# Performance work log

Hardware: AMD Instinct MI355X
Metric: run time of the kernel (lower is better)

## Reference

```python
import jax, jax.numpy as jnp
import numpy as np
import math

C = 512
D = C // 4  # 128
SCALE = math.sqrt(D)

def setup_inputs() -> dict:
    key = jax.random.key(0)
    k1, k2, k3, k4 = jax.random.split(key, 4)
    x = jax.random.normal(k1, (8, C, 2048), dtype=jnp.float32)
    # q_conv and k_conv share the same weight (tied in the torch module)
    wqk = jax.random.normal(k2, (D, C), dtype=jnp.float32) * (1.0 / math.sqrt(C))
    wv = jax.random.normal(k3, (D, C), dtype=jnp.float32) * (1.0 / math.sqrt(C))
    bv = jax.random.normal(k4, (D,), dtype=jnp.float32) * 0.01
    return {"x": x, "wqk": wqk, "wv": wv, "bv": bv}

def reference(x, wqk, wv, bv):
    # x: [B, C, N]; 1x1 conv == matmul over channel dim
    xq = jnp.einsum('dc,bcn->bnd', wqk, x)          # [B, N, D]
    xk = jnp.einsum('dc,bcn->bdn', wqk, x)          # [B, D, N]
    xv = jnp.einsum('dc,bcn->bdn', wv, x) + bv[None, :, None]  # [B, D, N]
    energy = jnp.einsum('bnd,bdm->bnm', xq, xk) / SCALE  # [B, N, N]
    attention = jax.nn.softmax(energy, axis=-1)
    x_r = jnp.einsum('bdn,bnm->bdm', xv, attention)  # [B, D, N]
    return x_r
```

## Files before the change

### kernel.cpp

```cpp
#include <hip/hip_runtime.h>

typedef short short4v __attribute__((ext_vector_type(4)));
typedef short short8 __attribute__((ext_vector_type(8)));
typedef float floatx4 __attribute__((ext_vector_type(4)));
typedef unsigned int uint;
typedef unsigned short ushort;

#define CH 512
#define NN 2048
#define DD 128
#define RSCALE 0.08838834764831845f

__device__ __forceinline__ float bf2f(ushort u) {
    union { uint i; float f; } v; v.i = ((uint)u) << 16; return v.f;
}
__device__ __forceinline__ ushort f2bf(float f) {
    union { float f; uint u; } v; v.f = f;
    uint u = v.u;
    return (ushort)((u + 0x7fffu + ((u >> 16) & 1u)) >> 16);
}

__global__ void k0_zero(float* __restrict__ lsum) {
    lsum[blockIdx.x * 256 + threadIdx.x] = 0.0f;
}

__global__ __launch_bounds__(256) void k0_wconv(
    const float* __restrict__ wqk, const float* __restrict__ wv,
    ushort* __restrict__ Wbf)
{
    int gid = blockIdx.x * 256 + threadIdx.x;
    int base = gid * 4;
    const float* src = (base < 65536) ? (wqk + base) : (wv + base - 65536);
    float4 v = *(const float4*)src;
    short4v o;
    o[0] = (short)f2bf(v.x); o[1] = (short)f2bf(v.y);
    o[2] = (short)f2bf(v.z); o[3] = (short)f2bf(v.w);
    *(short4v*)&Wbf[base] = o;
}

__global__ __launch_bounds__(256) void k1_proj(
    const float* __restrict__ x,
    const ushort* __restrict__ Wbf,
    const float* __restrict__ bv,
    ushort* __restrict__ Q,
    ushort* __restrict__ V)
{
    const int nt = blockIdx.x;
    const int b  = blockIdx.y;
    const int n0 = nt * 32;
    const int t = threadIdx.x;
    const int lane = t & 63, w = t >> 6, l15 = lane & 15, quad = lane >> 4;

    __shared__ __attribute__((aligned(16))) ushort As[32 * 40];
    __shared__ __attribute__((aligned(16))) ushort Bs[256 * 40];

    floatx4 acc[2][4];
#pragma unroll
    for (int i = 0; i < 2; i++)
#pragma unroll
        for (int j = 0; j < 4; j++) acc[i][j] = (floatx4)(0.0f);

    const float* xb = x + b * (CH * NN) + n0;

    for (int c0 = 0; c0 < CH; c0 += 32) {
        {
            int n = t & 31, g = t >> 5;
            short4v v;
#pragma unroll
            for (int i = 0; i < 4; i++)
                v[i] = (short)f2bf(xb[(c0 + g * 4 + i) * NN + n]);
            *(short4v*)&As[n * 40 + g * 4] = v;
        }
#pragma unroll
        for (int rep = 0; rep < 16; rep++) {
            int idx = rep * 256 + t;
            int row = idx >> 4, cp = idx & 15;
            *(uint*)&Bs[row * 40 + cp * 2] = *(const uint*)&Wbf[row * CH + c0 + cp * 2];
        }
        __syncthreads();
        short8 a0 = *(short8*)&As[(l15) * 40 + quad * 8];
        short8 a1 = *(short8*)&As[(16 + l15) * 40 + quad * 8];
#pragma unroll
        for (int dt2 = 0; dt2 < 4; dt2++) {
            short8 bf = *(short8*)&Bs[(w * 64 + dt2 * 16 + l15) * 40 + quad * 8];
            acc[0][dt2] = __builtin_amdgcn_mfma_f32_16x16x32_bf16(a0, bf, acc[0][dt2], 0, 0, 0);
            acc[1][dt2] = __builtin_amdgcn_mfma_f32_16x16x32_bf16(a1, bf, acc[1][dt2], 0, 0, 0);
        }
        __syncthreads();
    }
#pragma unroll
    for (int ns = 0; ns < 2; ns++)
#pragma unroll
        for (int dt2 = 0; dt2 < 4; dt2++) {
            int ds_ = w * 64 + dt2 * 16 + l15;
#pragma unroll
            for (int r = 0; r < 4; r++) {
                int n = n0 + ns * 16 + quad * 4 + r;
                float val = acc[ns][dt2][r];
                if (ds_ < 128) {
                    Q[b * (NN * DD) + n * DD + ds_] = f2bf(val);
                } else {
                    int dv = ds_ - 128;
                    V[b * (NN * DD) + n * DD + dv] = f2bf(val + bv[dv]);
                }
            }
        }
}

__global__ __launch_bounds__(256) void k2_qqt(
    const ushort* __restrict__ Q,
    ushort* __restrict__ Pg,
    float* __restrict__ lsum)
{
    const int it = blockIdx.x;
    const int jt = blockIdx.y;
    const int b  = blockIdx.z;
    const int i0 = it * 128, j0 = jt * 64;
    const int t = threadIdx.x;
    const int lane = t & 63, w = t >> 6, l15 = lane & 15, quad = lane >> 4;
    const int wi = (w >> 1) * 64, wj = (w & 1) * 32;

    __shared__ __attribute__((aligned(16))) ushort Qi[128 * 136];
    __shared__ __attribute__((aligned(16))) ushort Qj[64 * 136];

    const ushort* Qb = Q + b * (NN * DD);

#pragma unroll
    for (int rep = 0; rep < 8; rep++) {
        int idx = rep * 256 + t;
        int row = idx >> 4, g = idx & 15;
        *(short8*)&Qi[row * 136 + g * 8] = *(const short8*)&Qb[(i0 + row) * DD + g * 8];
    }
#pragma unroll
    for (int rep = 0; rep < 4; rep++) {
        int idx = rep * 256 + t;
        int row = idx >> 4, g = idx & 15;
        *(short8*)&Qj[row * 136 + g * 8] = *(const short8*)&Qb[(j0 + row) * DD + g * 8];
    }
    __syncthreads();

    floatx4 acc[4][2];
#pragma unroll
    for (int i = 0; i < 4; i++)
#pragma unroll
        for (int j = 0; j < 2; j++) acc[i][j] = (floatx4)(0.0f);

#pragma unroll
    for (int kd = 0; kd < 4; kd++) {
        short8 afr[4], bfr[2];
#pragma unroll
        for (int nt = 0; nt < 4; nt++)
            afr[nt] = *(short8*)&Qi[(wi + nt * 16 + l15) * 136 + kd * 32 + quad * 8];
#pragma unroll
        for (int mt = 0; mt < 2; mt++)
            bfr[mt] = *(short8*)&Qj[(wj + mt * 16 + l15) * 136 + kd * 32 + quad * 8];
#pragma unroll
        for (int nt = 0; nt < 4; nt++)
#pragma unroll
            for (int mt = 0; mt < 2; mt++)
                acc[nt][mt] = __builtin_amdgcn_mfma_f32_16x16x32_bf16(afr[nt], bfr[mt], acc[nt][mt], 0, 0, 0);
    }

    ushort* Pb = Pg + (size_t)b * NN * NN;
#pragma unroll
    for (int nt = 0; nt < 4; nt++) {
        float rs[4] = {0.f, 0.f, 0.f, 0.f};
#pragma unroll
        for (int mt = 0; mt < 2; mt++) {
#pragma unroll
            for (int r = 0; r < 4; r++) {
                float p = __expf(acc[nt][mt][r] * RSCALE);
                rs[r] += p;
                Pb[(size_t)(i0 + wi + nt * 16 + quad * 4 + r) * NN + (j0 + wj + mt * 16 + l15)] = f2bf(p);
            }
        }
#pragma unroll
        for (int r = 0; r < 4; r++) {
            float s = rs[r];
            s += __shfl_xor(s, 1);
            s += __shfl_xor(s, 2);
            s += __shfl_xor(s, 4);
            s += __shfl_xor(s, 8);
            if (l15 == 0)
                atomicAdd(&lsum[b * NN + i0 + wi + nt * 16 + quad * 4 + r], s);
        }
    }
}

__global__ __launch_bounds__(256) void k2_scale_t(
    const ushort* __restrict__ V,
    const float* __restrict__ lsum,
    ushort* __restrict__ VT)
{
    const int nt = blockIdx.x;
    const int b = blockIdx.y;
    const int n0 = nt * 64;
    const int t = threadIdx.x;

    __shared__ __attribute__((aligned(16))) ushort Vt[64 * 132];

    const ushort* Vb = V + b * (NN * DD);
#pragma unroll
    for (int rep = 0; rep < 16; rep++) {
        int idx = rep * 256 + t;
        int row = idx >> 6, dp = idx & 63;
        *(uint*)&Vt[row * 132 + dp * 2] = *(const uint*)&Vb[(n0 + row) * DD + dp * 2];
    }
    __syncthreads();
#pragma unroll
    for (int rep = 0; rep < 16; rep++) {
        int idx = rep * 256 + t;
        int d = idx >> 5, col2 = idx & 31;
        int n = n0 + col2 * 2;
        float l0 = 1.0f / lsum[b * NN + n], l1 = 1.0f / lsum[b * NN + n + 1];
        float v0 = bf2f(Vt[(col2 * 2) * 132 + d]) * l0;
        float v1 = bf2f(Vt[(col2 * 2 + 1) * 132 + d]) * l1;
        uint pack = (uint)f2bf(v0) | ((uint)f2bf(v1) << 16);
        *(uint*)&VT[(size_t)b * DD * NN + (size_t)d * NN + n] = pack;
    }
}

__global__ __launch_bounds__(256) void k3_gemm(
    const ushort* __restrict__ VT,
    const ushort* __restrict__ Pg,
    float* __restrict__ out)
{
    const int mt2 = blockIdx.x;
    const int b = blockIdx.y;
    const int m0 = mt2 * 32;
    const int t = threadIdx.x;
    const int lane = t & 63, w = t >> 6, l15 = lane & 15, quad = lane >> 4;

    __shared__ __attribute__((aligned(16))) ushort As2[128 * 72];
    __shared__ __attribute__((aligned(16))) ushort Ps2[32 * 72];

    const ushort* VTb = VT + (size_t)b * DD * NN;
    const ushort* Pb = Pg + (size_t)b * NN * NN;

    floatx4 acc[2][2];
#pragma unroll
    for (int i = 0; i < 2; i++)
#pragma unroll
        for (int j = 0; j < 2; j++) acc[i][j] = (floatx4)(0.0f);

    for (int n0c = 0; n0c < NN; n0c += 64) {
#pragma unroll
        for (int rep = 0; rep < 16; rep++) {
            int idx = rep * 256 + t;
            int row = idx >> 5, col2 = idx & 31;
            *(uint*)&As2[row * 72 + col2 * 2] = *(const uint*)&VTb[(size_t)row * NN + n0c + col2 * 2];
        }
#pragma unroll
        for (int rep = 0; rep < 4; rep++) {
            int idx = rep * 256 + t;
            int row = idx >> 5, col2 = idx & 31;
            *(uint*)&Ps2[row * 72 + col2 * 2] = *(const uint*)&Pb[(size_t)(m0 + row) * NN + n0c + col2 * 2];
        }
        __syncthreads();
#pragma unroll
        for (int kn = 0; kn < 2; kn++) {
            short8 pb0 = *(short8*)&Ps2[(l15) * 72 + kn * 32 + quad * 8];
            short8 pb1 = *(short8*)&Ps2[(16 + l15) * 72 + kn * 32 + quad * 8];
#pragma unroll
            for (int sub = 0; sub < 2; sub++) {
                short8 va = *(short8*)&As2[(w * 32 + sub * 16 + l15) * 72 + kn * 32 + quad * 8];
                acc[sub][0] = __builtin_amdgcn_mfma_f32_16x16x32_bf16(va, pb0, acc[sub][0], 0, 0, 0);
                acc[sub][1] = __builtin_amdgcn_mfma_f32_16x16x32_bf16(va, pb1, acc[sub][1], 0, 0, 0);
            }
        }
        __syncthreads();
    }

    float* ob = out + (size_t)b * DD * NN;
#pragma unroll
    for (int sub = 0; sub < 2; sub++)
#pragma unroll
        for (int mtk = 0; mtk < 2; mtk++)
#pragma unroll
            for (int r = 0; r < 4; r++) {
                int d = w * 32 + sub * 16 + quad * 4 + r;
                int m = m0 + mtk * 16 + l15;
                ob[(size_t)d * NN + m] = acc[sub][mtk][r];
            }
}

__global__ __launch_bounds__(256) void k1_fb(
    const float* __restrict__ x, const float* __restrict__ wqk,
    const float* __restrict__ wv, const float* __restrict__ bv,
    ushort* __restrict__ Q, ushort* __restrict__ V)
{
    const int nt = blockIdx.x;
    const int b  = blockIdx.y;
    const int n0 = nt * 32;
    const int t = threadIdx.x;
    const int lane = t & 63, w = t >> 6, l15 = lane & 15, quad = lane >> 4;

    __shared__ __attribute__((aligned(16))) ushort As[32 * 40];
    __shared__ __attribute__((aligned(16))) ushort Bs[256 * 40];

    floatx4 acc[2][4];
#pragma unroll
    for (int i = 0; i < 2; i++)
#pragma unroll
        for (int j = 0; j < 4; j++) acc[i][j] = (floatx4)(0.0f);

    const float* xb = x + b * (CH * NN) + n0;

    for (int c0 = 0; c0 < CH; c0 += 32) {
        {
            int n = t & 31, g = t >> 5;
            short4v v;
#pragma unroll
            for (int i = 0; i < 4; i++)
                v[i] = (short)f2bf(xb[(c0 + g * 4 + i) * NN + n]);
            *(short4v*)&As[n * 40 + g * 4] = v;
        }
#pragma unroll
        for (int rep = 0; rep < 16; rep++) {
            int idx = rep * 256 + t;
            int row = idx >> 4, cp = idx & 15;
            const float* wf = (row < 128) ? (wqk + row * CH) : (wv + (row - 128) * CH);
            uint pack = (uint)f2bf(wf[c0 + cp * 2]) | ((uint)f2bf(wf[c0 + cp * 2 + 1]) << 16);
            *(uint*)&Bs[row * 40 + cp * 2] = pack;
        }
        __syncthreads();
        short8 a0 = *(short8*)&As[(l15) * 40 + quad * 8];
        short8 a1 = *(short8*)&As[(16 + l15) * 40 + quad * 8];
#pragma unroll
        for (int dt2 = 0; dt2 < 4; dt2++) {
            short8 bf = *(short8*)&Bs[(w * 64 + dt2 * 16 + l15) * 40 + quad * 8];
            acc[0][dt2] = __builtin_amdgcn_mfma_f32_16x16x32_bf16(a0, bf, acc[0][dt2], 0, 0, 0);
            acc[1][dt2] = __builtin_amdgcn_mfma_f32_16x16x32_bf16(a1, bf, acc[1][dt2], 0, 0, 0);
        }
        __syncthreads();
    }
#pragma unroll
    for (int ns = 0; ns < 2; ns++)
#pragma unroll
        for (int dt2 = 0; dt2 < 4; dt2++) {
            int ds_ = w * 64 + dt2 * 16 + l15;
#pragma unroll
            for (int r = 0; r < 4; r++) {
                int n = n0 + ns * 16 + quad * 4 + r;
                float val = acc[ns][dt2][r];
                if (ds_ < 128) {
                    Q[b * (NN * DD) + n * DD + ds_] = f2bf(val);
                } else {
                    int dv = ds_ - 128;
                    V[b * (NN * DD) + n * DD + dv] = f2bf(val + bv[dv]);
                }
            }
        }
}

__global__ __launch_bounds__(256) void k2_norm(
    const ushort* __restrict__ Q, ushort* __restrict__ V)
{
    const int ntile = blockIdx.x;
    const int b = blockIdx.y;
    const int n0 = ntile * 64;
    const int t = threadIdx.x;
    const int lane = t & 63, w = t >> 6, l15 = lane & 15, quad = lane >> 4;

    __shared__ __attribute__((aligned(16))) ushort Qs[64 * 136];
    __shared__ __attribute__((aligned(16))) ushort Qm[64 * 136];

    const ushort* Qb = Q + b * (NN * DD);

#pragma unroll
    for (int rep = 0; rep < 16; rep++) {
        int idx = rep * 256 + t;
        int row = idx >> 6, dp = idx & 63;
        *(uint*)&Qs[row * 136 + dp * 2] = *(const uint*)&Qb[(n0 + row) * DD + dp * 2];
    }
    __syncthreads();

    short8 afr[4];
#pragma unroll
    for (int kd = 0; kd < 4; kd++)
        afr[kd] = *(short8*)&Qs[(w * 16 + l15) * 136 + kd * 32 + quad * 8];

    float sums[4] = {0.f, 0.f, 0.f, 0.f};

    for (int m0 = 0; m0 < NN; m0 += 64) {
#pragma unroll
        for (int rep = 0; rep < 16; rep++) {
            int idx = rep * 256 + t;
            int row = idx >> 6, dp = idx & 63;
            *(uint*)&Qm[row * 136 + dp * 2] = *(const uint*)&Qb[(m0 + row) * DD + dp * 2];
        }
        __syncthreads();
#pragma unroll
        for (int ct = 0; ct < 4; ct++) {
            floatx4 s = (floatx4)(0.0f);
#pragma unroll
            for (int kd = 0; kd < 4; kd++) {
                short8 bf = *(short8*)&Qm[(ct * 16 + l15) * 136 + kd * 32 + quad * 8];
                s = __builtin_amdgcn_mfma_f32_16x16x32_bf16(afr[kd], bf, s, 0, 0, 0);
            }
#pragma unroll
            for (int r = 0; r < 4; r++)
                sums[r] += __expf(s[r] * RSCALE);
        }
        __syncthreads();
    }

#pragma unroll
    for (int r = 0; r < 4; r++) {
        float s = sums[r];
        s += __shfl_xor(s, 1);
        s += __shfl_xor(s, 2);
        s += __shfl_xor(s, 4);
        s += __shfl_xor(s, 8);
        sums[r] = s;
    }

    ushort* Vb = V + b * (NN * DD);
#pragma unroll
    for (int r = 0; r < 4; r++) {
        int n = n0 + w * 16 + quad * 4 + r;
        float inv = 1.0f / sums[r];
        short8 vv = *(short8*)&Vb[n * DD + l15 * 8];
        short8 o;
#pragma unroll
        for (int i = 0; i < 8; i++)
            o[i] = (short)f2bf(bf2f((ushort)vv[i]) * inv);
        *(short8*)&Vb[n * DD + l15 * 8] = o;
    }
}

__global__ __launch_bounds__(256) void k3_attn(
    const ushort* __restrict__ Q, const ushort* __restrict__ Vp,
    float* __restrict__ out)
{
    const int mtile = blockIdx.x;
    const int b = blockIdx.y;
    const int m0 = mtile * 64;
    const int t = threadIdx.x;
    const int lane = t & 63, w = t >> 6, l15 = lane & 15, quad = lane >> 4;

    __shared__ __attribute__((aligned(16))) ushort Qs[64 * 136];
    __shared__ __attribute__((aligned(16))) ushort Qn[32 * 136];
    __shared__ __attribute__((aligned(16))) ushort Vs[128 * 40];
    __shared__ __attribute__((aligned(16))) ushort Ps[64 * 40];

    const ushort* Qb = Q + b * (NN * DD);
    const ushort* Vpb = Vp + b * (NN * DD);

#pragma unroll
    for (int rep = 0; rep < 16; rep++) {
        int idx = rep * 256 + t;
        int row = idx >> 6, dp = idx & 63;
        *(uint*)&Qs[row * 136 + dp * 2] = *(const uint*)&Qb[(m0 + row) * DD + dp * 2];
    }
    __syncthreads();

    short8 afr[4];
#pragma unroll
    for (int kd = 0; kd < 4; kd++)
        afr[kd] = *(short8*)&Qs[(w * 16 + l15) * 136 + kd * 32 + quad * 8];

    floatx4 acc[2][4];
#pragma unroll
    for (int s = 0; s < 2; s++)
#pragma unroll
        for (int mt = 0; mt < 4; mt++) acc[s][mt] = (floatx4)(0.0f);

    for (int n0c = 0; n0c < NN; n0c += 32) {
#pragma unroll
        for (int rep = 0; rep < 8; rep++) {
            int idx = rep * 256 + t;
            int row = idx >> 6, dp = idx & 63;
            *(uint*)&Qn[row * 136 + dp * 2] = *(const uint*)&Qb[(n0c + row) * DD + dp * 2];
        }
#pragma unroll
        for (int rep = 0; rep < 8; rep++) {
            int idx = rep * 256 + t;
            int np = idx >> 7, d = idx & 127;
            uint v0 = Vpb[(n0c + np * 2) * DD + d];
            uint v1 = Vpb[(n0c + np * 2 + 1) * DD + d];
            *(uint*)&Vs[d * 40 + np * 2] = v0 | (v1 << 16);
        }
        __syncthreads();

#pragma unroll
        for (int nt2 = 0; nt2 < 2; nt2++) {
            floatx4 s = (floatx4)(0.0f);
#pragma unroll
            for (int kd = 0; kd < 4; kd++) {
                short8 bf = *(short8*)&Qn[(nt2 * 16 + l15) * 136 + kd * 32 + quad * 8];
                s = __builtin_amdgcn_mfma_f32_16x16x32_bf16(afr[kd], bf, s, 0, 0, 0);
            }
#pragma unroll
            for (int r = 0; r < 4; r++) {
                float p = __expf(s[r] * RSCALE);
                Ps[(w * 16 + quad * 4 + r) * 40 + nt2 * 16 + l15] = f2bf(p);
            }
        }
        __syncthreads();

        short8 pb[4];
#pragma unroll
        for (int mt = 0; mt < 4; mt++)
            pb[mt] = *(short8*)&Ps[(mt * 16 + l15) * 40 + quad * 8];
#pragma unroll
        for (int sub = 0; sub < 2; sub++) {
            short8 va = *(short8*)&Vs[(w * 32 + sub * 16 + l15) * 40 + quad * 8];
#pragma unroll
            for (int mt = 0; mt < 4; mt++)
                acc[sub][mt] = __builtin_amdgcn_mfma_f32_16x16x32_bf16(va, pb[mt], acc[sub][mt], 0, 0, 0);
        }
        __syncthreads();
    }

    float* ob = out + (size_t)b * DD * NN;
#pragma unroll
    for (int sub = 0; sub < 2; sub++)
#pragma unroll
        for (int mt = 0; mt < 4; mt++)
#pragma unroll
            for (int r = 0; r < 4; r++) {
                int d = w * 32 + sub * 16 + quad * 4 + r;
                int m = m0 + mt * 16 + l15;
                ob[(size_t)d * NN + m] = acc[sub][mt][r];
            }
}

extern "C" void kernel_launch(void* const* d_in, const int* in_sizes, int n_in,
                              void* d_out, int out_size, void* d_ws, size_t ws_size,
                              hipStream_t stream) {
    const float* x   = (const float*)d_in[0];
    const float* wqk = (const float*)d_in[1];
    const float* wv  = (const float*)d_in[2];
    const float* bv  = (const float*)d_in[3];
    float* out = (float*)d_out;

    ushort* Q = (ushort*)d_ws;
    ushort* V = (ushort*)((char*)d_ws + (4u << 20));

    if (ws_size >= (size_t)80 * 1024 * 1024) {
        ushort* Wbf  = (ushort*)((char*)d_ws + (8u << 20));
        float*  lsum = (float*)((char*)d_ws + (8u << 20) + (256u << 10));
        ushort* VT   = (ushort*)((char*)d_ws + (12u << 20));
        ushort* Pg   = (ushort*)((char*)d_ws + (16u << 20));

        k0_zero<<<64, 256, 0, stream>>>(lsum);
        k0_wconv<<<128, 256, 0, stream>>>(wqk, wv, Wbf);
        k1_proj<<<dim3(64, 8), 256, 0, stream>>>(x, Wbf, bv, Q, V);
        k2_qqt<<<dim3(16, 32, 8), 256, 0, stream>>>(Q, Pg, lsum);
        k2_scale_t<<<dim3(32, 8), 256, 0, stream>>>(V, lsum, VT);
        k3_gemm<<<dim3(64, 8), 256, 0, stream>>>(VT, Pg, out);
    } else {
        k1_fb<<<dim3(64, 8), 256, 0, stream>>>(x, wqk, wv, bv, Q, V);
        k2_norm<<<dim3(32, 8), 256, 0, stream>>>(Q, V);
        k3_attn<<<dim3(32, 8), 256, 0, stream>>>(Q, V, out);
    }
}
```

Baseline: 182.0 us.

## Recompute exp(QQ^T) in fused PV kernel instead of materializing P

The row-sum kernel now only computes the softmax normalizers and no longer writes the full bf16 probability matrix (8x2048x2048) to global memory. The final GEMM kernel recomputes the Q·Q^T tile and its exponentials on the fly in shared memory and multiplies them by the pre-scaled V^T, which avoids the large write and read-back of P. The cost is computing the energy matmul and exp twice. The workspace threshold for the fast path drops because the P buffer is gone.

New measurement: 191.7 us. 5.3% more time.

```diff
diff --git a/kernel.cpp b/kernel.cpp
--- a/kernel.cpp
+++ b/kernel.cpp
@@ -107,9 +107,8 @@
         }
 }
 
-__global__ __launch_bounds__(256) void k2_qqt(
+__global__ __launch_bounds__(256) void kl_sum(
     const ushort* __restrict__ Q,
-    ushort* __restrict__ Pg,
     float* __restrict__ lsum)
 {
     const int it = blockIdx.x;
@@ -161,19 +160,14 @@
                 acc[nt][mt] = __builtin_amdgcn_mfma_f32_16x16x32_bf16(afr[nt], bfr[mt], acc[nt][mt], 0, 0, 0);
     }
 
-    ushort* Pb = Pg + (size_t)b * NN * NN;
 #pragma unroll
     for (int nt = 0; nt < 4; nt++) {
         float rs[4] = {0.f, 0.f, 0.f, 0.f};
 #pragma unroll
-        for (int mt = 0; mt < 2; mt++) {
-#pragma unroll
-            for (int r = 0; r < 4; r++) {
-                float p = __expf(acc[nt][mt][r] * RSCALE);
-                rs[r] += p;
-                Pb[(size_t)(i0 + wi + nt * 16 + quad * 4 + r) * NN + (j0 + wj + mt * 16 + l15)] = f2bf(p);
-            }
-        }
+        for (int mt = 0; mt < 2; mt++)
+#pragma unroll
+            for (int r = 0; r < 4; r++)
+                rs[r] += __expf(acc[nt][mt][r] * RSCALE);
 #pragma unroll
         for (int r = 0; r < 4; r++) {
             float s = rs[r];
@@ -220,22 +214,39 @@
     }
 }
 
-__global__ __launch_bounds__(256) void k3_gemm(
+__global__ __launch_bounds__(256) void k_fused(
+    const ushort* __restrict__ Q,
     const ushort* __restrict__ VT,
-    const ushort* __restrict__ Pg,
     float* __restrict__ out)
 {
-    const int mt2 = blockIdx.x;
+    const int mt = blockIdx.x;
     const int b = blockIdx.y;
-    const int m0 = mt2 * 32;
+    const int m0 = mt * 32;
     const int t = threadIdx.x;
     const int lane = t & 63, w = t >> 6, l15 = lane & 15, quad = lane >> 4;
 
-    __shared__ __attribute__((aligned(16))) ushort As2[128 * 72];
-    __shared__ __attribute__((aligned(16))) ushort Ps2[32 * 72];
-
+    __shared__ __attribute__((aligned(16))) ushort Qm[32 * 136];
+    __shared__ __attribute__((aligned(16))) ushort Qn[64 * 136];
+    __shared__ __attribute__((aligned(16))) ushort Vs[128 * 72];
+    __shared__ __attribute__((aligned(16))) ushort Ps[32 * 68];
+
+    const ushort* Qb = Q + b * (NN * DD);
     const ushort* VTb = VT + (size_t)b * DD * NN;
-    const ushort* Pb = Pg + (size_t)b * NN * NN;
+
+#pragma unroll
+    for (int rep = 0; rep < 2; rep++) {
+        int idx = rep * 256 + t;
+        int row = idx >> 4, g = idx & 15;
+        *(short8*)&Qm[row * 136 + g * 8] = *(const short8*)&Qb[(m0 + row) * DD + g * 8];
+    }
+    __syncthreads();
+
+    short8 qm[2][4];
+#pragma unroll
+    for (int ms = 0; ms < 2; ms++)
+#pragma unroll
+        for (int kd = 0; kd < 4; kd++)
+            qm[ms][kd] = *(short8*)&Qm[(ms * 16 + l15) * 136 + kd * 32 + quad * 8];
 
     floatx4 acc[2][2];
 #pragma unroll
@@ -244,44 +255,59 @@
         for (int j = 0; j < 2; j++) acc[i][j] = (floatx4)(0.0f);
 
     for (int n0c = 0; n0c < NN; n0c += 64) {
-#pragma unroll
-        for (int rep = 0; rep < 16; rep++) {
-            int idx = rep * 256 + t;
-            int row = idx >> 5, col2 = idx & 31;
-            *(uint*)&As2[row * 72 + col2 * 2] = *(const uint*)&VTb[(size_t)row * NN + n0c + col2 * 2];
-        }
+        __syncthreads();
 #pragma unroll
         for (int rep = 0; rep < 4; rep++) {
             int idx = rep * 256 + t;
-            int row = idx >> 5, col2 = idx & 31;
-            *(uint*)&Ps2[row * 72 + col2 * 2] = *(const uint*)&Pb[(size_t)(m0 + row) * NN + n0c + col2 * 2];
-        }
-        __syncthreads();
+            int row = idx >> 4, g = idx & 15;
+            *(short8*)&Qn[row * 136 + g * 8] = *(const short8*)&Qb[(n0c + row) * DD + g * 8];
+        }
+#pragma unroll
+        for (int rep = 0; rep < 4; rep++) {
+            int idx = rep * 256 + t;
+            int d = idx >> 3, g = idx & 7;
+            *(short8*)&Vs[d * 72 + g * 8] = *(const short8*)&VTb[(size_t)d * NN + n0c + g * 8];
+        }
+        __syncthreads();
+
+#pragma unroll
+        for (int ms = 0; ms < 2; ms++) {
+            floatx4 s = (floatx4)(0.0f);
+#pragma unroll
+            for (int kd = 0; kd < 4; kd++) {
+                short8 bq = *(short8*)&Qn[(w * 16 + l15) * 136 + kd * 32 + quad * 8];
+                s = __builtin_amdgcn_mfma_f32_16x16x32_bf16(qm[ms][kd], bq, s, 0, 0, 0);
+            }
+#pragma unroll
+            for (int r = 0; r < 4; r++) {
+                float p = __expf(s[r] * RSCALE);
+                Ps[(ms * 16 + quad * 4 + r) * 68 + w * 16 + l15] = f2bf(p);
+            }
+        }
+        __syncthreads();
+
 #pragma unroll
         for (int kn = 0; kn < 2; kn++) {
-            short8 pb0 = *(short8*)&Ps2[(l15) * 72 + kn * 32 + quad * 8];
-            short8 pb1 = *(short8*)&Ps2[(16 + l15) * 72 + kn * 32 + quad * 8];
-#pragma unroll
-            for (int sub = 0; sub < 2; sub++) {
-                short8 va = *(short8*)&As2[(w * 32 + sub * 16 + l15) * 72 + kn * 32 + quad * 8];
-                acc[sub][0] = __builtin_amdgcn_mfma_f32_16x16x32_bf16(va, pb0, acc[sub][0], 0, 0, 0);
-                acc[sub][1] = __builtin_amdgcn_mfma_f32_16x16x32_bf16(va, pb1, acc[sub][1], 0, 0, 0);
-            }
-        }
-        __syncthreads();
+            short8 va0 = *(short8*)&Vs[(w * 32 + l15) * 72 + kn * 32 + quad * 8];
+            short8 va1 = *(short8*)&Vs[(w * 32 + 16 + l15) * 72 + kn * 32 + quad * 8];
+            short8 pb0 = *(short8*)&Ps[(l15) * 68 + kn * 32 + quad * 8];
+            short8 pb1 = *(short8*)&Ps[(16 + l15) * 68 + kn * 32 + quad * 8];
+            acc[0][0] = __builtin_amdgcn_mfma_f32_16x16x32_bf16(va0, pb0, acc[0][0], 0, 0, 0);
+            acc[0][1] = __builtin_amdgcn_mfma_f32_16x16x32_bf16(va0, pb1, acc[0][1], 0, 0, 0);
+            acc[1][0] = __builtin_amdgcn_mfma_f32_16x16x32_bf16(va1, pb0, acc[1][0], 0, 0, 0);
+            acc[1][1] = __builtin_amdgcn_mfma_f32_16x16x32_bf16(va1, pb1, acc[1][1], 0, 0, 0);
+        }
     }
 
     float* ob = out + (size_t)b * DD * NN;
 #pragma unroll
-    for (int sub = 0; sub < 2; sub++)
-#pragma unroll
-        for (int mtk = 0; mtk < 2; mtk++)
-#pragma unroll
-            for (int r = 0; r < 4; r++) {
-                int d = w * 32 + sub * 16 + quad * 4 + r;
-                int m = m0 + mtk * 16 + l15;
-                ob[(size_t)d * NN + m] = acc[sub][mtk][r];
-            }
+    for (int dsub = 0; dsub < 2; dsub++)
+#pragma unroll
+        for (int r = 0; r < 4; r++) {
+            int d = w * 32 + dsub * 16 + quad * 4 + r;
+            ob[(size_t)d * NN + m0 + l15]      = acc[dsub][0][r];
+            ob[(size_t)d * NN + m0 + 16 + l15] = acc[dsub][1][r];
+        }
 }
 
 __global__ __launch_bounds__(256) void k1_fb(
@@ -363,7 +389,7 @@
     const int lane = t & 63, w = t >> 6, l15 = lane & 15, quad = lane >> 4;
 
     __shared__ __attribute__((aligned(16))) ushort Qs[64 * 136];
-    __shared__ __attribute__((aligned(16))) ushort Qm[64 * 136];
+    __shared__ __attribute__((aligned(16))) ushort Qm2[64 * 136];
 
     const ushort* Qb = Q + b * (NN * DD);
 
@@ -387,7 +413,7 @@
         for (int rep = 0; rep < 16; rep++) {
             int idx = rep * 256 + t;
             int row = idx >> 6, dp = idx & 63;
-            *(uint*)&Qm[row * 136 + dp * 2] = *(const uint*)&Qb[(m0 + row) * DD + dp * 2];
+            *(uint*)&Qm2[row * 136 + dp * 2] = *(const uint*)&Qb[(m0 + row) * DD + dp * 2];
         }
         __syncthreads();
 #pragma unroll
@@ -395,7 +421,7 @@
             floatx4 s = (floatx4)(0.0f);
 #pragma unroll
             for (int kd = 0; kd < 4; kd++) {
-                short8 bf = *(short8*)&Qm[(ct * 16 + l15) * 136 + kd * 32 + quad * 8];
+                short8 bf = *(short8*)&Qm2[(ct * 16 + l15) * 136 + kd * 32 + quad * 8];
                 s = __builtin_amdgcn_mfma_f32_16x16x32_bf16(afr[kd], bf, s, 0, 0, 0);
             }
 #pragma unroll
@@ -440,9 +466,9 @@
     const int lane = t & 63, w = t >> 6, l15 = lane & 15, quad = lane >> 4;
 
     __shared__ __attribute__((aligned(16))) ushort Qs[64 * 136];
-    __shared__ __attribute__((aligned(16))) ushort Qn[32 * 136];
-    __shared__ __attribute__((aligned(16))) ushort Vs[128 * 40];
-    __shared__ __attribute__((aligned(16))) ushort Ps[64 * 40];
+    __shared__ __attribute__((aligned(16))) ushort Qn2[32 * 136];
+    __shared__ __attribute__((aligned(16))) ushort Vs2[128 * 40];
+    __shared__ __attribute__((aligned(16))) ushort Ps2[64 * 40];
 
     const ushort* Qb = Q + b * (NN * DD);
     const ushort* Vpb = Vp + b * (NN * DD);
@@ -471,7 +497,7 @@
         for (int rep = 0; rep < 8; rep++) {
             int idx = rep * 256 + t;
             int row = idx >> 6, dp = idx & 63;
-            *(uint*)&Qn[row * 136 + dp * 2] = *(const uint*)&Qb[(n0c + row) * DD + dp * 2];
+            *(uint*)&Qn2[row * 136 + dp * 2] = *(const uint*)&Qb[(n0c + row) * DD + dp * 2];
         }
 #pragma unroll
         for (int rep = 0; rep < 8; rep++) {
@@ -479,7 +505,7 @@
             int np = idx >> 7, d = idx & 127;
             uint v0 = Vpb[(n0c + np * 2) * DD + d];
             uint v1 = Vpb[(n0c + np * 2 + 1) * DD + d];
-            *(uint*)&Vs[d * 40 + np * 2] = v0 | (v1 << 16);
+            *(uint*)&Vs2[d * 40 + np * 2] = v0 | (v1 << 16);
         }
         __syncthreads();
 
@@ -488,13 +514,13 @@
             floatx4 s = (floatx4)(0.0f);
 #pragma unroll
             for (int kd = 0; kd < 4; kd++) {
-                short8 bf = *(short8*)&Qn[(nt2 * 16 + l15) * 136 + kd * 32 + quad * 8];
+                short8 bf = *(short8*)&Qn2[(nt2 * 16 + l15) * 136 + kd * 32 + quad * 8];
                 s = __builtin_amdgcn_mfma_f32_16x16x32_bf16(afr[kd], bf, s, 0, 0, 0);
             }
 #pragma unroll
             for (int r = 0; r < 4; r++) {
                 float p = __expf(s[r] * RSCALE);
-                Ps[(w * 16 + quad * 4 + r) * 40 + nt2 * 16 + l15] = f2bf(p);
+                Ps2[(w * 16 + quad * 4 + r) * 40 + nt2 * 16 + l15] = f2bf(p);
             }
         }
         __syncthreads();
@@ -502,10 +528,10 @@
         short8 pb[4];
 #pragma unroll
         for (int mt = 0; mt < 4; mt++)
-            pb[mt] = *(short8*)&Ps[(mt * 16 + l15) * 40 + quad * 8];
+            pb[mt] = *(short8*)&Ps2[(mt * 16 + l15) * 40 + quad * 8];
 #pragma unroll
         for (int sub = 0; sub < 2; sub++) {
-            short8 va = *(short8*)&Vs[(w * 32 + sub * 16 + l15) * 40 + quad * 8];
+            short8 va = *(short8*)&Vs2[(w * 32 + sub * 16 + l15) * 40 + quad * 8];
 #pragma unroll
             for (int mt = 0; mt < 4; mt++)
                 acc[sub][mt] = __builtin_amdgcn_mfma_f32_16x16x32_bf16(va, pb[mt], acc[sub][mt], 0, 0, 0);
@@ -538,18 +564,17 @@
     ushort* Q = (ushort*)d_ws;
     ushort* V = (ushort*)((char*)d_ws + (4u << 20));
 
-    if (ws_size >= (size_t)80 * 1024 * 1024) {
+    if (ws_size >= (size_t)16 * 1024 * 1024) {
         ushort* Wbf  = (ushort*)((char*)d_ws + (8u << 20));
         float*  lsum = (float*)((char*)d_ws + (8u << 20) + (256u << 10));
         ushort* VT   = (ushort*)((char*)d_ws + (12u << 20));
-        ushort* Pg   = (ushort*)((char*)d_ws + (16u << 20));
 
         k0_zero<<<64, 256, 0, stream>>>(lsum);
         k0_wconv<<<128, 256, 0, stream>>>(wqk, wv, Wbf);
         k1_proj<<<dim3(64, 8), 256, 0, stream>>>(x, Wbf, bv, Q, V);
-        k2_qqt<<<dim3(16, 32, 8), 256, 0, stream>>>(Q, Pg, lsum);
+        kl_sum<<<dim3(16, 32, 8), 256, 0, stream>>>(Q, lsum);
         k2_scale_t<<<dim3(32, 8), 256, 0, stream>>>(V, lsum, VT);
-        k3_gemm<<<dim3(64, 8), 256, 0, stream>>>(VT, Pg, out);
+        k_fused<<<dim3(64, 8), 256, 0, stream>>>(Q, VT, out);
     } else {
         k1_fb<<<dim3(64, 8), 256, 0, stream>>>(x, wqk, wv, bv, Q, V);
         k2_norm<<<dim3(32, 8), 256, 0, stream>>>(Q, V);
```
